# Optimization experiments

Hardware: AMD Instinct MI355X
Metric: run time of the kernel (lower is better)

The kernel has to match this reference:

```python
import jax, jax.numpy as jnp
import numpy as np

NODE_DIM = 8
IN_EDGE_DIM = 4
OUT_EDGE_DIM = 4
HID = 16
N_NODES = 100000
N_EDGES = 3200000
LN_EPS = 1e-5


def _layer_norm(h, gamma, beta):
    mu = jnp.mean(h, axis=-1, keepdims=True)
    var = jnp.mean(jnp.square(h - mu), axis=-1, keepdims=True)
    return (h - mu) * jax.lax.rsqrt(var + LN_EPS) * gamma + beta


def setup_inputs() -> dict:
    key = jax.random.key(0)
    ks = jax.random.split(key, 12)
    in_dim = NODE_DIM * 2 + IN_EDGE_DIM  # 20
    x = jax.random.normal(ks[0], (N_NODES, NODE_DIM), dtype=jnp.float32)
    edge_index = jax.random.randint(ks[1], (2, N_EDGES), 0, N_NODES, dtype=jnp.int64)
    edge_attr = jax.random.normal(ks[2], (N_EDGES, IN_EDGE_DIM), dtype=jnp.float32)
    # MLP params (Kaiming-uniform-ish scaling like torch defaults)
    def lin(k, fan_in, fan_out):
        lim = 1.0 / np.sqrt(fan_in)
        kw, kb = jax.random.split(k)
        W = jax.random.uniform(kw, (fan_in, fan_out), minval=-lim, maxval=lim, dtype=jnp.float32)
        b = jax.random.uniform(kb, (fan_out,), minval=-lim, maxval=lim, dtype=jnp.float32)
        return W, b
    W1, b1 = lin(ks[3], in_dim, HID)
    W2, b2 = lin(ks[4], HID, HID)
    W3, b3 = lin(ks[5], HID, OUT_EDGE_DIM)
    g1 = jnp.ones((HID,), jnp.float32); be1 = jnp.zeros((HID,), jnp.float32)
    g2 = jnp.ones((HID,), jnp.float32); be2 = jnp.zeros((HID,), jnp.float32)
    return {"x": x, "edge_index": edge_index, "edge_attr": edge_attr,
            "W1": W1, "b1": b1, "g1": g1, "be1": be1,
            "W2": W2, "b2": b2, "g2": g2, "be2": be2,
            "W3": W3, "b3": b3}


def reference(x, edge_index, edge_attr, W1, b1, g1, be1, W2, b2, g2, be2, W3, b3):
    frm = edge_index[0]
    to = edge_index[1]
    # gather node features for both endpoints, concat with edge features: [E, 2*node_dim+in_edge_dim]
    inpt = jnp.concatenate([x[frm], x[to], edge_attr.astype(jnp.float32)], axis=1)
    h = _layer_norm(jax.nn.relu(inpt @ W1 + b1), g1, be1)
    h = _layer_norm(jax.nn.relu(h @ W2 + b2), g2, be2)
    return h @ W3 + b3  # [E, out_edge_dim]
```

## Files before the change

### kernel.cpp

```cpp
#include <hip/hip_runtime.h>
#include <stdint.h>


using u16 = unsigned short;
using u32 = uint32_t;
typedef float v2f __attribute__((ext_vector_type(2)));

__device__ __forceinline__ v2f v2fma(v2f a, v2f b, v2f c) {
    return __builtin_elementwise_fma(a, b, c);
}
__device__ __forceinline__ v2f v2max0(v2f a) {
    v2f z = {0.f, 0.f};
    return __builtin_elementwise_max(a, z);
}

__device__ __forceinline__ float bf2f(u16 u) { return __uint_as_float(((u32)u) << 16); }
__device__ __forceinline__ float bflo(u32 u) { return __uint_as_float(u << 16); }
__device__ __forceinline__ float bfhi(u32 u) { return __uint_as_float(u & 0xFFFF0000u); }
__device__ __forceinline__ u32 f2bf(float f) {
    u32 u = __float_as_uint(f);
    return (u + 0x7FFFu + ((u >> 16) & 1u)) >> 16;
}
__device__ __forceinline__ float ldw(const void* p, int i, bool bf) {
    return bf ? bf2f(((const u16*)p)[i]) : ((const float*)p)[i];
}

#define WB_W1 0
#define WB_B1 320
#define WB_W2 336
#define WB_B2 592
#define WB_W3 608
#define WB_B3 672
#define WB_TOT 704
#define WV_W1 0
#define WV_B1 160
#define WV_W2 168
#define WV_B2 296
#define WV_W3 304
#define WV_B3 336

__global__ __launch_bounds__(256)
void probe_convert(const int* __restrict__ ei, int n_pairs,
                   const void* W1, const void* b1, const void* g1, const void* be1,
                   const void* W2, const void* b2, const void* g2, const void* be2,
                   const void* W3, const void* b3,
                   int* __restrict__ flags, float* __restrict__ wb) {
    bool bf = (((const u32*)g1)[0] == 0x3F803F80u);
    __shared__ int s;
    if (threadIdx.x == 0) s = 0;
    __syncthreads();
    int limit = n_pairs < 2048 ? n_pairs : 2048;
    int found = 0;
    for (int i = threadIdx.x; i < limit; i += blockDim.x)
        if (ei[2 * i + 1] != 0) found = 1;
    if (found) s = 1;
    __syncthreads();
    if (threadIdx.x == 0) { flags[0] = s; flags[1] = bf ? 1 : 0; }

    int t = threadIdx.x;
    for (int i = t; i < 320; i += 256) wb[WB_W1 + i] = ldw(W1, i, bf);
    if (t < 16) wb[WB_B1 + t] = ldw(b1, t, bf);
    {
        int k = t >> 4;
        wb[WB_W2 + t] = ldw(g1, k, bf) * ldw(W2, t, bf);
    }
    if (t < 16) {
        float acc = ldw(b2, t, bf);
        for (int k = 0; k < 16; k++) acc = fmaf(ldw(be1, k, bf), ldw(W2, k * 16 + t, bf), acc);
        wb[WB_B2 + t] = acc;
    }
    if (t < 64) {
        int k = t >> 2;
        wb[WB_W3 + t] = ldw(g2, k, bf) * ldw(W3, t, bf);
    }
    if (t < 4) {
        float acc = ldw(b3, t, bf);
        for (int k = 0; k < 16; k++) acc = fmaf(ldw(be2, k, bf), ldw(W3, k * 4 + t, bf), acc);
        wb[WB_B3 + t] = acc;
    }
    if (t >= 4 && t < 32) wb[672 + t] = 0.f;
}

__device__ __forceinline__ void relu_ln8v(v2f* h) {
    v2f sv = {0.f, 0.f}, qv = {0.f, 0.f};
#pragma unroll
    for (int p = 0; p < 8; p++) {
        h[p] = v2max0(h[p]);
        sv += h[p];
        qv = v2fma(h[p], h[p], qv);
    }
    float s = sv.x + sv.y, q = qv.x + qv.y;
    float mu = s * 0.0625f;
    float var = fmaf(-mu, mu, q * 0.0625f);
    float r = rsqrtf(var + 1e-5f);
    float n = -mu * r;
    v2f rv = {r, r}, nv = {n, n};
#pragma unroll
    for (int p = 0; p < 8; p++) h[p] = v2fma(h[p], rv, nv);
}

__device__ __forceinline__ void rows4(v2f* h, const v2f* __restrict__ wv,
                                      float4 v, int base) {
    float c[4] = {v.x, v.y, v.z, v.w};
#pragma unroll
    for (int t = 0; t < 4; t++) {
        const v2f* w = wv + WV_W1 + (base + t) * 8;
        v2f a = {c[t], c[t]};
#pragma unroll
        for (int p = 0; p < 8; p++) h[p] = v2fma(a, w[p], h[p]);
    }
}

__device__ __forceinline__ float4 bfq_lo(uint4 r) {
    return make_float4(bflo(r.x), bfhi(r.x), bflo(r.y), bfhi(r.y));
}
__device__ __forceinline__ float4 bfq_hi(uint4 r) {
    return make_float4(bflo(r.z), bfhi(r.z), bflo(r.w), bfhi(r.w));
}

__global__ __launch_bounds__(256)
void edge_mlp(const void* __restrict__ x, const int* __restrict__ ei,
              const void* __restrict__ ea, const float* __restrict__ wb,
              const int* __restrict__ flags, void* __restrict__ out, int n_edges) {
    const v2f* wv = (const v2f*)wb;

    const bool idx32 = flags[0] != 0;
    const bool bf = flags[1] != 0;

    int e = blockIdx.x * 256 + threadIdx.x;
    if (e >= n_edges) return;

    int frm, to;
    if (idx32) {
        frm = ei[e];
        to  = ei[n_edges + e];
    } else {
        frm = ei[2 * (size_t)e];
        to  = ei[2 * ((size_t)n_edges + e)];
    }

    v2f h[8];
#pragma unroll
    for (int p = 0; p < 8; p++) h[p] = wv[WV_B1 + p];

    if (bf) {
        uint4 a = ((const uint4*)x)[frm];
        rows4(h, wv, bfq_lo(a), 0);
        rows4(h, wv, bfq_hi(a), 4);
        uint4 c = ((const uint4*)x)[to];
        rows4(h, wv, bfq_lo(c), 8);
        rows4(h, wv, bfq_hi(c), 12);
        uint2 r = ((const uint2*)ea)[e];
        rows4(h, wv, make_float4(bflo(r.x), bfhi(r.x), bflo(r.y), bfhi(r.y)), 16);
    } else {
        const float4* xp = (const float4*)x;
        float4 xa = xp[2 * frm], xb = xp[2 * frm + 1];
        float4 xc = xp[2 * to],  xd = xp[2 * to + 1];
        float4 ev = ((const float4*)ea)[e];
        rows4(h, wv, xa, 0);
        rows4(h, wv, xb, 4);
        rows4(h, wv, xc, 8);
        rows4(h, wv, xd, 12);
        rows4(h, wv, ev, 16);
    }

    relu_ln8v(h);

    v2f av[8];
#pragma unroll
    for (int p = 0; p < 8; p++) av[p] = wv[WV_B2 + p];
#pragma unroll
    for (int k = 0; k < 16; k++) {
        float z = (k & 1) ? h[k >> 1].y : h[k >> 1].x;
        v2f zb = {z, z};
        const v2f* w = wv + WV_W2 + k * 8;
#pragma unroll
        for (int p = 0; p < 8; p++) av[p] = v2fma(zb, w[p], av[p]);
    }

    relu_ln8v(av);

    v2f oa = wv[WV_B3 + 0], ob = wv[WV_B3 + 1];
#pragma unroll
    for (int k = 0; k < 16; k++) {
        float z = (k & 1) ? av[k >> 1].y : av[k >> 1].x;
        v2f zb = {z, z};
        oa = v2fma(zb, wv[WV_W3 + k * 2], oa);
        ob = v2fma(zb, wv[WV_W3 + k * 2 + 1], ob);
    }

    if (bf) {
        uint2 p;
        p.x = f2bf(oa.x) | (f2bf(oa.y) << 16);
        p.y = f2bf(ob.x) | (f2bf(ob.y) << 16);
        ((uint2*)out)[e] = p;
    } else {
        ((float4*)out)[e] = make_float4(oa.x, oa.y, ob.x, ob.y);
    }
}

extern "C" void kernel_launch(void* const* d_in, const int* in_sizes, int n_in,
                              void* d_out, int out_size, void* d_ws, size_t ws_size,
                              hipStream_t stream) {
    const void* x  = d_in[0];
    const int* ei  = (const int*)d_in[1];
    const void* ea = d_in[2];

    int n_edges = in_sizes[1] / 2;

    int* flags = (int*)d_ws;
    float* wb = (float*)((char*)d_ws + 64);

    probe_convert<<<1, 256, 0, stream>>>(ei, n_edges,
                                         d_in[3], d_in[4], d_in[5], d_in[6],
                                         d_in[7], d_in[8], d_in[9], d_in[10],
                                         d_in[11], d_in[12], flags, wb);

    int eblocks = (n_edges + 255) / 256;
    edge_mlp<<<eblocks, 256, 0, stream>>>(x, ei, ea, wb, flags, d_out, n_edges);
}
```

Before: 192.6 us.

## Compute bf16 edge MLP with MFMA 16x16x32 tiles and split-precision weights

Adds an MFMA kernel for the bf16 path. Each wavefront handles 16-edge tiles, and the three linear layers run as bf16 matrix-core ops. Layers two and three use a hi/lo bf16 split of weights and activations to keep accuracy. LayerNorm reductions go through cross-lane shuffles, and activations are redistributed into MFMA operand layout with shuffles. The scalar fp32 FMA kernel stays as the fp32 fallback; both kernels are always launched and each exits early based on the dtype flag. This adds an extra launch plus shuffle overhead per tile, and accuracy depends on the split-bf16 approximation.

Measured after the change: 205.2 us. 1.07x slower.

```diff
diff --git a/kernel.cpp b/kernel.cpp
--- a/kernel.cpp
+++ b/kernel.cpp
@@ -5,6 +5,9 @@
 using u16 = unsigned short;
 using u32 = uint32_t;
 typedef float v2f __attribute__((ext_vector_type(2)));
+typedef __attribute__((ext_vector_type(4))) float f32x4;
+typedef __attribute__((ext_vector_type(8))) short bf16x8;
+typedef __attribute__((ext_vector_type(2))) __bf16 bf16x2;
 
 __device__ __forceinline__ v2f v2fma(v2f a, v2f b, v2f c) {
     return __builtin_elementwise_fma(a, b, c);
@@ -20,6 +23,12 @@
 __device__ __forceinline__ u32 f2bf(float f) {
     u32 u = __float_as_uint(f);
     return (u + 0x7FFFu + ((u >> 16) & 1u)) >> 16;
+}
+__device__ __forceinline__ u32 pkbf(float a, float b) {
+    bf16x2 t;
+    t.x = (__bf16)a;
+    t.y = (__bf16)b;
+    return __builtin_bit_cast(u32, t);
 }
 __device__ __forceinline__ float ldw(const void* p, int i, bool bf) {
     return bf ? bf2f(((const u16*)p)[i]) : ((const float*)p)[i];
@@ -38,6 +47,12 @@
 #define WV_B2 296
 #define WV_W3 304
 #define WV_B3 336
+#define FQ_A1 0
+#define FQ_A2H 512
+#define FQ_A2L 1024
+#define FQ_A3H 1536
+#define FQ_A3L 2048
+#define FB_OFF (WB_TOT + 1280)
 
 __global__ __launch_bounds__(256)
 void probe_convert(const int* __restrict__ ei, int n_pairs,
@@ -79,6 +94,152 @@
         wb[WB_B3 + t] = acc;
     }
     if (t >= 4 && t < 32) wb[672 + t] = 0.f;
+
+    __syncthreads();
+
+    u16* fq = (u16*)(wb + WB_TOT);
+    for (int i = t; i < 512; i += 256) {
+        int l = i >> 3, j = i & 7;
+        int m = l & 15, g = l >> 4;
+        int k = g * 8 + j;
+        int kk = k & 15;
+        fq[FQ_A1 + i] = (u16)f2bf(k < 20 ? wb[WB_W1 + k * 16 + m] : 0.f);
+        float w2 = wb[WB_W2 + kk * 16 + m];
+        u16 h2 = (u16)f2bf(w2);
+        fq[FQ_A2H + i] = h2;
+        fq[FQ_A2L + i] = (u16)f2bf(w2 - bf2f(h2));
+        float w3 = (m < 4) ? wb[WB_W3 + kk * 4 + m] : 0.f;
+        u16 h3 = (u16)f2bf(w3);
+        fq[FQ_A3H + i] = h3;
+        fq[FQ_A3L + i] = (u16)f2bf(w3 - bf2f(h3));
+    }
+    {
+        float* fbv = wb + FB_OFF;
+        int l = t >> 2, r = t & 3;
+        int row = ((l >> 4) << 2) + r;
+        fbv[t] = wb[WB_B1 + row];
+        fbv[256 + t] = wb[WB_B2 + row];
+        fbv[512 + t] = (row < 4) ? wb[WB_B3 + row] : 0.f;
+    }
+}
+
+__device__ __forceinline__ void ln16(f32x4 d, float& h0, float& h1, float& h2, float& h3) {
+    f32x4 z = {0.f, 0.f, 0.f, 0.f};
+    d = __builtin_elementwise_max(d, z);
+    float s = (d.x + d.y) + (d.z + d.w);
+    float q = fmaf(d.x, d.x, fmaf(d.y, d.y, fmaf(d.z, d.z, d.w * d.w)));
+    s += __shfl_xor(s, 16);
+    q += __shfl_xor(q, 16);
+    s += __shfl_xor(s, 32);
+    q += __shfl_xor(q, 32);
+    float mu = s * 0.0625f;
+    float var = fmaf(-mu, mu, q * 0.0625f);
+    float r = rsqrtf(var + 1e-5f);
+    float nb = -mu * r;
+    h0 = fmaf(d.x, r, nb);
+    h1 = fmaf(d.y, r, nb);
+    h2 = fmaf(d.z, r, nb);
+    h3 = fmaf(d.w, r, nb);
+}
+
+__device__ __forceinline__ bf16x8 redist_split(float h0, float h1, float h2, float h3,
+                                               int n, int g) {
+    u32 hi01 = pkbf(h0, h1), hi23 = pkbf(h2, h3);
+    float r0 = h0 - bflo(hi01);
+    float r1 = h1 - bfhi(hi01);
+    float r2 = h2 - bflo(hi23);
+    float r3 = h3 - bfhi(hi23);
+    u32 lo01 = pkbf(r0, r1), lo23 = pkbf(r2, r3);
+    int srcA = n + (((g & 1) << 1) << 4);
+    int srcB = srcA + 16;
+    u32 hA01 = (u32)__shfl((int)hi01, srcA);
+    u32 hA23 = (u32)__shfl((int)hi23, srcA);
+    u32 lA01 = (u32)__shfl((int)lo01, srcA);
+    u32 lA23 = (u32)__shfl((int)lo23, srcA);
+    u32 hB01 = (u32)__shfl((int)hi01, srcB);
+    u32 hB23 = (u32)__shfl((int)hi23, srcB);
+    u32 lB01 = (u32)__shfl((int)lo01, srcB);
+    u32 lB23 = (u32)__shfl((int)lo23, srcB);
+    bool hi = (g < 2);
+    uint4 uu = make_uint4(hi ? hA01 : lA01, hi ? hA23 : lA23,
+                          hi ? hB01 : lB01, hi ? hB23 : lB23);
+    return __builtin_bit_cast(bf16x8, uu);
+}
+
+#define TPW 8
+
+__global__ __launch_bounds__(256, 6)
+void edge_mlp_mfma(const void* __restrict__ x, const int* __restrict__ ei,
+                   const void* __restrict__ ea, const float* __restrict__ wb,
+                   const int* __restrict__ flags, void* __restrict__ out, int n_edges) {
+    if (flags[1] == 0) return;
+    const bool idx32 = flags[0] != 0;
+
+    const int lane = threadIdx.x & 63;
+    const int n = lane & 15;
+    const int g = lane >> 4;
+
+    const u16* fq = (const u16*)(wb + WB_TOT);
+    bf16x8 A1  = ((const bf16x8*)fq)[lane];
+    bf16x8 A2h = ((const bf16x8*)fq)[64 + lane];
+    bf16x8 A2l = ((const bf16x8*)fq)[128 + lane];
+    bf16x8 A3h = ((const bf16x8*)fq)[192 + lane];
+    bf16x8 A3l = ((const bf16x8*)fq)[256 + lane];
+    const f32x4* fb = (const f32x4*)(wb + FB_OFF);
+    f32x4 pb1 = fb[lane];
+    f32x4 pb2 = fb[64 + lane];
+    f32x4 pb3 = fb[128 + lane];
+
+    const int ntiles = (n_edges + 15) >> 4;
+    const int wflat = blockIdx.x * 4 + (threadIdx.x >> 6);
+    const int t0 = wflat * TPW;
+
+#pragma unroll 1
+    for (int ti = 0; ti < TPW; ++ti) {
+        int tile = t0 + ti;
+        if (tile >= ntiles) break;
+
+        int e = (tile << 4) + n;
+        bool ev = e < n_edges;
+
+        uint4 raw = make_uint4(0u, 0u, 0u, 0u);
+        if (g < 2) {
+            size_t col = (g == 0) ? (size_t)e : ((size_t)n_edges + (size_t)e);
+            int idx = 0;
+            if (ev) idx = idx32 ? ei[col] : ei[2 * col];
+            raw = ((const uint4*)x)[idx];
+        } else if (g == 2) {
+            if (ev) {
+                uint2 r = ((const uint2*)ea)[e];
+                raw.x = r.x;
+                raw.y = r.y;
+            }
+        }
+
+        f32x4 d1 = pb1;
+        d1 = __builtin_amdgcn_mfma_f32_16x16x32_bf16(A1, __builtin_bit_cast(bf16x8, raw),
+                                                     d1, 0, 0, 0);
+        float h0, h1, h2, h3;
+        ln16(d1, h0, h1, h2, h3);
+
+        bf16x8 f2 = redist_split(h0, h1, h2, h3, n, g);
+        f32x4 d2 = pb2;
+        d2 = __builtin_amdgcn_mfma_f32_16x16x32_bf16(A2h, f2, d2, 0, 0, 0);
+        d2 = __builtin_amdgcn_mfma_f32_16x16x32_bf16(A2l, f2, d2, 0, 0, 0);
+        float z0, z1, z2, z3;
+        ln16(d2, z0, z1, z2, z3);
+
+        bf16x8 f3 = redist_split(z0, z1, z2, z3, n, g);
+        f32x4 d3 = pb3;
+        d3 = __builtin_amdgcn_mfma_f32_16x16x32_bf16(A3h, f3, d3, 0, 0, 0);
+        d3 = __builtin_amdgcn_mfma_f32_16x16x32_bf16(A3l, f3, d3, 0, 0, 0);
+
+        if (g == 0 && ev) {
+            u32 p0 = pkbf(d3.x, d3.y);
+            u32 p1 = pkbf(d3.z, d3.w);
+            ((uint2*)out)[e] = make_uint2(p0, p1);
+        }
+    }
 }
 
 __device__ __forceinline__ void relu_ln8v(v2f* h) {
@@ -111,21 +272,13 @@
     }
 }
 
-__device__ __forceinline__ float4 bfq_lo(uint4 r) {
-    return make_float4(bflo(r.x), bfhi(r.x), bflo(r.y), bfhi(r.y));
-}
-__device__ __forceinline__ float4 bfq_hi(uint4 r) {
-    return make_float4(bflo(r.z), bfhi(r.z), bflo(r.w), bfhi(r.w));
-}
-
 __global__ __launch_bounds__(256)
 void edge_mlp(const void* __restrict__ x, const int* __restrict__ ei,
               const void* __restrict__ ea, const float* __restrict__ wb,
               const int* __restrict__ flags, void* __restrict__ out, int n_edges) {
+    if (flags[1] != 0) return;
     const v2f* wv = (const v2f*)wb;
-
     const bool idx32 = flags[0] != 0;
-    const bool bf = flags[1] != 0;
 
     int e = blockIdx.x * 256 + threadIdx.x;
     if (e >= n_edges) return;
@@ -143,26 +296,15 @@
 #pragma unroll
     for (int p = 0; p < 8; p++) h[p] = wv[WV_B1 + p];
 
-    if (bf) {
-        uint4 a = ((const uint4*)x)[frm];
-        rows4(h, wv, bfq_lo(a), 0);
-        rows4(h, wv, bfq_hi(a), 4);
-        uint4 c = ((const uint4*)x)[to];
-        rows4(h, wv, bfq_lo(c), 8);
-        rows4(h, wv, bfq_hi(c), 12);
-        uint2 r = ((const uint2*)ea)[e];
-        rows4(h, wv, make_float4(bflo(r.x), bfhi(r.x), bflo(r.y), bfhi(r.y)), 16);
-    } else {
-        const float4* xp = (const float4*)x;
-        float4 xa = xp[2 * frm], xb = xp[2 * frm + 1];
-        float4 xc = xp[2 * to],  xd = xp[2 * to + 1];
-        float4 ev = ((const float4*)ea)[e];
-        rows4(h, wv, xa, 0);
-        rows4(h, wv, xb, 4);
-        rows4(h, wv, xc, 8);
-        rows4(h, wv, xd, 12);
-        rows4(h, wv, ev, 16);
-    }
+    const float4* xp = (const float4*)x;
+    float4 xa = xp[2 * frm], xb = xp[2 * frm + 1];
+    float4 xc = xp[2 * to],  xd = xp[2 * to + 1];
+    float4 evv = ((const float4*)ea)[e];
+    rows4(h, wv, xa, 0);
+    rows4(h, wv, xb, 4);
+    rows4(h, wv, xc, 8);
+    rows4(h, wv, xd, 12);
+    rows4(h, wv, evv, 16);
 
     relu_ln8v(h);
 
@@ -189,14 +331,7 @@
         ob = v2fma(zb, wv[WV_W3 + k * 2 + 1], ob);
     }
 
-    if (bf) {
-        uint2 p;
-        p.x = f2bf(oa.x) | (f2bf(oa.y) << 16);
-        p.y = f2bf(ob.x) | (f2bf(ob.y) << 16);
-        ((uint2*)out)[e] = p;
-    } else {
-        ((float4*)out)[e] = make_float4(oa.x, oa.y, ob.x, ob.y);
-    }
+    ((float4*)out)[e] = make_float4(oa.x, oa.y, ob.x, ob.y);
 }
 
 extern "C" void kernel_launch(void* const* d_in, const int* in_sizes, int n_in,
@@ -216,6 +351,10 @@
                                          d_in[7], d_in[8], d_in[9], d_in[10],
                                          d_in[11], d_in[12], flags, wb);
 
+    int ntiles = (n_edges + 15) / 16;
+    int mblocks = (ntiles + 4 * TPW - 1) / (4 * TPW);
+    edge_mlp_mfma<<<mblocks, 256, 0, stream>>>(x, ei, ea, wb, flags, d_out, n_edges);
+
     int eblocks = (n_edges + 255) / 256;
     edge_mlp<<<eblocks, 256, 0, stream>>>(x, ei, ea, wb, flags, d_out, n_edges);
 }
```
